# Optimization experiments

Hardware: AMD Instinct MI355X
Metric: run time of the kernel (lower is better)

The kernel has to match this reference:

```python
import jax, jax.numpy as jnp
import numpy as np

L = 5          # num_layers
N = 50000      # nodes
E = 600000     # edges
D = 128        # num_features == hidden_units
G = 256        # graphs in batch
O = 10         # num_outputs
BN_EPS = 1e-5


def setup_inputs() -> dict:
    key = jax.random.key(0)
    ks = jax.random.split(key, 8)
    x = jax.random.normal(ks[0], (N, D), jnp.float32)
    edge_index = jax.random.randint(ks[1], (2, E), 0, N, jnp.int32)
    edge_attr = jax.random.randint(ks[2], (E, 3), 0, 8, jnp.int32)
    batch = jnp.sort(jax.random.randint(ks[3], (N,), 0, G, jnp.int32))
    s = 0.05
    return {
        "x": x,
        "edge_index": edge_index,
        "edge_attr": edge_attr,
        "batch": batch,
        "bond_emb": jax.random.normal(ks[4], (L, 3, 8, D), jnp.float32) * s,
        "conv_w1": jax.random.normal(ks[5], (L, D, D), jnp.float32) * s,
        "conv_b1": jnp.zeros((L, D), jnp.float32),
        "conv_bn_gamma": jnp.ones((L, D), jnp.float32),
        "conv_bn_beta": jnp.zeros((L, D), jnp.float32),
        "conv_bn_mean": jnp.zeros((L, D), jnp.float32),
        "conv_bn_var": jnp.ones((L, D), jnp.float32),
        "conv_w2": jax.random.normal(ks[6], (L, D, D), jnp.float32) * s,
        "conv_b2": jnp.zeros((L, D), jnp.float32),
        "bn_gamma": jnp.ones((L, D), jnp.float32),
        "bn_beta": jnp.zeros((L, D), jnp.float32),
        "bn_mean": jnp.zeros((L, D), jnp.float32),
        "bn_var": jnp.ones((L, D), jnp.float32),
        "fc_w": jax.random.normal(ks[7], (L + 1, D, O), jnp.float32) * s,
        "fc_b": jnp.zeros((L + 1, O), jnp.float32),
    }


def _bn_eval(h, gamma, beta, mean, var):
    return (h - mean) * jax.lax.rsqrt(var + BN_EPS) * gamma + beta


def reference(x, edge_index, edge_attr, batch, bond_emb,
              conv_w1, conv_b1, conv_bn_gamma, conv_bn_beta, conv_bn_mean, conv_bn_var,
              conv_w2, conv_b2, bn_gamma, bn_beta, bn_mean, bn_var, fc_w, fc_b):
    src, dst = edge_index[0], edge_index[1]  # x_j = x[src], aggregate at dst
    feat_ids = jnp.arange(3)
    outs = [x]
    for i in range(L):
        # BondEncoder: sum of per-feature embeddings -> [E, D]
        ea = bond_emb[i][feat_ids, edge_attr].sum(axis=1)
        # GINEConv (eps=0): msg = relu(x_j + edge_attr), scatter-add, nn(x + aggr)
        msg = jax.nn.relu(x[src] + ea)
        aggr = jax.ops.segment_sum(msg, dst, num_segments=N)
        h = x + aggr
        h = h @ conv_w1[i] + conv_b1[i]
        h = jax.nn.relu(_bn_eval(h, conv_bn_gamma[i], conv_bn_beta[i], conv_bn_mean[i], conv_bn_var[i]))
        h = h @ conv_w2[i] + conv_b2[i]
        x = jax.nn.relu(_bn_eval(h, bn_gamma[i], bn_beta[i], bn_mean[i], bn_var[i]))
        outs.append(x)
    # global mean pool per layer output, linear head, sum (dropout = identity in eval)
    counts = jax.ops.segment_sum(jnp.ones((N,), x.dtype), batch, num_segments=G)
    inv = 1.0 / jnp.maximum(counts, 1.0)
    out = jnp.zeros((G, O), x.dtype)
    for i, h in enumerate(outs):
        pooled = jax.ops.segment_sum(h, batch, num_segments=G) * inv[:, None]
        out = out + pooled @ fc_w[i] + fc_b[i]
    return out
```

## Files before the change

kernel.cpp:

```cpp
#include <hip/hip_runtime.h>

#define NN 50000
#define EE 600000
#define DD 128
#define GG 256
#define LL 5
#define OO 10
#define BN_EPS 1e-5f
#define CPAD 513
#define ESTRIDE 40
#define SENT (512u << 16)

#define B_CVT   3125
#define B_COMBO 1283
#define B_WT    160
#define B_EFILL 1954
#define B_EPOS  196
#define B_INV   1
#define B_POOL0 391
#define B_PREP  (B_CVT + B_COMBO + B_WT + B_EFILL + B_EPOS + B_INV + B_POOL0)

typedef __attribute__((ext_vector_type(8))) short short8;
typedef __attribute__((ext_vector_type(16))) float float16;

__device__ __forceinline__ unsigned short f2b(float f) {
    unsigned u = __float_as_uint(f);
    unsigned r = u + 0x7FFFu + ((u >> 16) & 1u);
    return (unsigned short)(r >> 16);
}
__device__ __forceinline__ unsigned pk2(float lo, float hi) {
    return (unsigned)f2b(lo) | ((unsigned)f2b(hi) << 16);
}
__device__ __forceinline__ float blo(unsigned u) { return __uint_as_float(u << 16); }
__device__ __forceinline__ float bhi(unsigned u) { return __uint_as_float(u & 0xFFFF0000u); }

__launch_bounds__(256)
__global__ void prep(const float* __restrict__ x, const int* __restrict__ batch,
                     const float* __restrict__ bond,
                     const float* __restrict__ w1, const float* __restrict__ w2,
                     unsigned* __restrict__ xb4, unsigned short* __restrict__ combo,
                     short* __restrict__ wt, unsigned* __restrict__ e_info,
                     int* __restrict__ epos, float* __restrict__ inv,
                     float* __restrict__ pooled0) {
    const int bid = blockIdx.x, t = threadIdx.x;
    if (bid < B_CVT) {
        int gid = bid * 256 + t;
        const float4* xp = (const float4*)(x + (size_t)gid * 8);
        float4 a = xp[0], b = xp[1];
        uint4 o;
        o.x = pk2(a.x, a.y); o.y = pk2(a.z, a.w);
        o.z = pk2(b.x, b.y); o.w = pk2(b.z, b.w);
        ((uint4*)xb4)[gid] = o;
    } else if (bid < B_CVT + B_COMBO) {
        int e = (bid - B_CVT) * 256 + t;
        if (e < LL * CPAD * DD) {
            int l = e / (CPAD * DD), rem = e - l * (CPAD * DD);
            int c = rem / DD, d = rem - c * DD;
            float s;
            if (c == 512) s = -1e30f;
            else {
                const float* b_ = bond + (size_t)l * 3 * 8 * DD;
                s = b_[(c & 7) * DD + d] + b_[(8 + ((c >> 3) & 7)) * DD + d]
                  + b_[(16 + (c >> 6)) * DD + d];
            }
            combo[e] = f2b(s);
        }
    } else if (bid < B_CVT + B_COMBO + B_WT) {
        __shared__ float tile[32][33];
        int b = bid - B_CVT - B_COMBO;
        int mat = b >> 4, tl = b & 15;
        int k0 = (tl >> 2) * 32, c0 = (tl & 3) * 32;
        const float* W = (mat < 5) ? (w1 + (size_t)mat * DD * DD)
                                   : (w2 + (size_t)(mat - 5) * DD * DD);
        int j = t & 31, q = t >> 5;
#pragma unroll
        for (int rr = 0; rr < 4; ++rr) {
            int row = q + rr * 8;
            tile[row][j] = W[(size_t)(k0 + row) * DD + c0 + j];
        }
        __syncthreads();
#pragma unroll
        for (int rr = 0; rr < 4; ++rr) {
            int cr = q + rr * 8;
            wt[(size_t)mat * DD * DD + (size_t)(c0 + cr) * DD + k0 + j] = (short)f2b(tile[j][cr]);
        }
    } else if (bid < B_CVT + B_COMBO + B_WT + B_EFILL) {
        int gid = (bid - B_CVT - B_COMBO - B_WT) * 256 + t;
        if (gid < NN * ESTRIDE / 4)
            ((uint4*)e_info)[gid] = make_uint4(SENT, SENT, SENT, SENT);
    } else if (bid < B_CVT + B_COMBO + B_WT + B_EFILL + B_EPOS) {
        int n = (bid - B_CVT - B_COMBO - B_WT - B_EFILL) * 256 + t;
        if (n < NN) epos[n] = n * ESTRIDE;
    } else if (bid < B_CVT + B_COMBO + B_WT + B_EFILL + B_EPOS + B_INV) {
        __shared__ int sg[GG + 1];
        int g = t, lo = 0, hi = NN;
        while (lo < hi) { int m = (lo + hi) >> 1; if (batch[m] < g) lo = m + 1; else hi = m; }
        sg[g] = lo;
        if (g == 0) sg[GG] = NN;
        __syncthreads();
        inv[g] = 1.0f / fmaxf((float)(sg[g + 1] - sg[g]), 1.0f);
    } else {
        int b = bid - (B_CVT + B_COMBO + B_WT + B_EFILL + B_EPOS + B_INV);
        int n0 = b * 128;
        __shared__ int sb[128];
        __shared__ float part[4][DD];
        if (t < 128) { int row = n0 + t; sb[t] = (row < NN) ? batch[row] : -1; }
        ((float*)part)[t] = 0.f;
        ((float*)part)[t + 256] = 0.f;
        __syncthreads();
        int gmin = sb[0];
        int col = t & 127, rh = t >> 7;
        float pg[4] = {0.f, 0.f, 0.f, 0.f};
        for (int r = rh; r < 128; r += 2) {
            int s = sb[r];
            float v = (s >= 0) ? x[(size_t)(n0 + r) * DD + col] : 0.f;
            int dg = s - gmin;
#pragma unroll
            for (int jj = 0; jj < 4; ++jj) pg[jj] += (dg == jj) ? v : 0.f;
        }
#pragma unroll
        for (int jj = 0; jj < 4; ++jj)
            if (pg[jj] != 0.f) atomicAdd(&part[jj][col], pg[jj]);
        __syncthreads();
        for (int q2 = t; q2 < 4 * DD; q2 += 256) {
            int jj = q2 >> 7, c2 = q2 & 127;
            float v = part[jj][c2];
            if (v != 0.f && gmin + jj < GG) atomicAdd(&pooled0[(gmin + jj) * DD + c2], v);
        }
    }
}

__launch_bounds__(256)
__global__ void scatter_edges(const int* __restrict__ ei, const int* __restrict__ eattr,
                              int* __restrict__ epos, unsigned* __restrict__ e_info) {
    int e = blockIdx.x * 256 + threadIdx.x;
    if (e >= EE) return;
    int dst = ei[EE + e];
    int pos = atomicAdd(&epos[dst], 1);
    unsigned cidx = (unsigned)eattr[e * 3 + 0] | ((unsigned)eattr[e * 3 + 1] << 3)
                  | ((unsigned)eattr[e * 3 + 2] << 6);
    e_info[pos] = (unsigned)ei[e] | (cidx << 16);
}

__launch_bounds__(256)
__global__ void aggr_csr(const unsigned short* __restrict__ xin,
                         const int* __restrict__ epos,
                         const unsigned* __restrict__ e_info,
                         const unsigned short* __restrict__ combo,
                         unsigned short* __restrict__ hin) {
    int node = blockIdx.x * 4 + (threadIdx.x >> 6);
    int lane = threadIdx.x & 63;
    if (node >= NN) return;
    const int base = node * ESTRIDE;
    const int deg  = epos[node] - base;
    const int pe   = base + ((deg + 7) & ~7);
    const int eg   = lane >> 4;
    const int f    = (lane & 15) * 8;
    float acc[8];
#pragma unroll
    for (int i = 0; i < 8; ++i) acc[i] = 0.f;

    for (int p = base; p < pe; p += 8) {
        unsigned i0 = e_info[p + eg];
        unsigned i1 = e_info[p + 4 + eg];
        uint4 xv0 = *(const uint4*)&xin[(size_t)(i0 & 0xFFFFu) * DD + f];
        uint4 cv0 = *(const uint4*)&combo[(size_t)(i0 >> 16) * DD + f];
        uint4 xv1 = *(const uint4*)&xin[(size_t)(i1 & 0xFFFFu) * DD + f];
        uint4 cv1 = *(const uint4*)&combo[(size_t)(i1 >> 16) * DD + f];
        acc[0] += fmaxf(blo(xv0.x) + blo(cv0.x), 0.f) + fmaxf(blo(xv1.x) + blo(cv1.x), 0.f);
        acc[1] += fmaxf(bhi(xv0.x) + bhi(cv0.x), 0.f) + fmaxf(bhi(xv1.x) + bhi(cv1.x), 0.f);
        acc[2] += fmaxf(blo(xv0.y) + blo(cv0.y), 0.f) + fmaxf(blo(xv1.y) + blo(cv1.y), 0.f);
        acc[3] += fmaxf(bhi(xv0.y) + bhi(cv0.y), 0.f) + fmaxf(bhi(xv1.y) + bhi(cv1.y), 0.f);
        acc[4] += fmaxf(blo(xv0.z) + blo(cv0.z), 0.f) + fmaxf(blo(xv1.z) + blo(cv1.z), 0.f);
        acc[5] += fmaxf(bhi(xv0.z) + bhi(cv0.z), 0.f) + fmaxf(bhi(xv1.z) + bhi(cv1.z), 0.f);
        acc[6] += fmaxf(blo(xv0.w) + blo(cv0.w), 0.f) + fmaxf(blo(xv1.w) + blo(cv1.w), 0.f);
        acc[7] += fmaxf(bhi(xv0.w) + bhi(cv0.w), 0.f) + fmaxf(bhi(xv1.w) + bhi(cv1.w), 0.f);
    }
#pragma unroll
    for (int i = 0; i < 8; ++i) {
        acc[i] += __shfl_xor(acc[i], 16, 64);
        acc[i] += __shfl_xor(acc[i], 32, 64);
    }
    if (lane < 16) {
        uint4 self = *(const uint4*)&xin[(size_t)node * DD + f];
        uint4 o;
        o.x = pk2(acc[0] + blo(self.x), acc[1] + bhi(self.x));
        o.y = pk2(acc[2] + blo(self.y), acc[3] + bhi(self.y));
        o.z = pk2(acc[4] + blo(self.z), acc[5] + bhi(self.z));
        o.w = pk2(acc[6] + blo(self.w), acc[7] + bhi(self.w));
        *(uint4*)&hin[(size_t)node * DD + f] = o;
    }
}

__launch_bounds__(256)
__global__ void conv_fused(const unsigned short* __restrict__ hin,
                           const short* __restrict__ Wt1, const short* __restrict__ Wt2,
                           const float* __restrict__ b1, const float* __restrict__ g1,
                           const float* __restrict__ be1, const float* __restrict__ m1,
                           const float* __restrict__ v1,
                           const float* __restrict__ b2, const float* __restrict__ g2,
                           const float* __restrict__ be2, const float* __restrict__ m2,
                           const float* __restrict__ v2,
                           const int* __restrict__ batch,
                           unsigned short* __restrict__ outb,
                           float* __restrict__ pool_slot) {
    __shared__ short As[64 * 136];
    __shared__ int sbg[64];
    const int tid  = threadIdx.x;
    const int lane = tid & 63;
    const int wave = tid >> 6;
    const int row0 = blockIdx.x * 64;

    const int col   = wave * 32 + (lane & 31);
    const int khalf = (lane >> 5) * 8;
    const int arow  = lane & 31;
    const int rbase = 4 * (lane >> 5);
    const int gmin  = batch[row0];

    short8 bf[8];
#pragma unroll
    for (int ch = 0; ch < 8; ++ch)
        bf[ch] = *(const short8*)&Wt1[col * DD + ch * 16 + khalf];

    const float sc1 = g1[col] * rsqrtf(v1[col] + BN_EPS);
    const float sh1 = fmaf(b1[col] - m1[col], sc1, be1[col]);
    const float sc2 = g2[col] * rsqrtf(v2[col] + BN_EPS);
    const float sh2 = fmaf(b2[col] - m2[col], sc2, be2[col]);

    if (tid < 64) {
        int row = row0 + tid;
        sbg[tid] = (row < NN) ? batch[row] - gmin : -1;
    }
    for (int i = tid; i < 1024; i += 256) {
        int r = i >> 4, c8 = (i & 15) * 8;
        int row = row0 + r;
        uint4 z = make_uint4(0, 0, 0, 0);
        if (row < NN) z = *(const uint4*)&hin[(size_t)row * DD + c8];
        *(uint4*)&As[r * 136 + c8] = z;
    }
    __syncthreads();

    float16 acc0 = {0.f,0.f,0.f,0.f,0.f,0.f,0.f,0.f,0.f,0.f,0.f,0.f,0.f,0.f,0.f,0.f};
    float16 acc1 = acc0;
#pragma unroll
    for (int ch = 0; ch < 8; ++ch) {
        short8 a0 = *(const short8*)&As[(arow     ) * 136 + ch * 16 + khalf];
        short8 a1 = *(const short8*)&As[(32 + arow) * 136 + ch * 16 + khalf];
        acc0 = __builtin_amdgcn_mfma_f32_32x32x16_bf16(a0, bf[ch], acc0, 0, 0, 0);
        acc1 = __builtin_amdgcn_mfma_f32_32x32x16_bf16(a1, bf[ch], acc1, 0, 0, 0);
    }

#pragma unroll
    for (int ch = 0; ch < 8; ++ch)
        bf[ch] = *(const short8*)&Wt2[col * DD + ch * 16 + khalf];

    __syncthreads();
#pragma unroll
    for (int r = 0; r < 16; ++r) {
        int rl = (r & 3) + 8 * (r >> 2) + rbase;
        As[rl * 136 + col]        = (short)f2b(fmaxf(fmaf(acc0[r], sc1, sh1), 0.f));
        As[(32 + rl) * 136 + col] = (short)f2b(fmaxf(fmaf(acc1[r], sc1, sh1), 0.f));
    }
    __syncthreads();

    acc0 = acc1 = float16{0.f,0.f,0.f,0.f,0.f,0.f,0.f,0.f,0.f,0.f,0.f,0.f,0.f,0.f,0.f,0.f};
#pragma unroll
    for (int ch = 0; ch < 8; ++ch) {
        short8 a0 = *(const short8*)&As[(arow     ) * 136 + ch * 16 + khalf];
        short8 a1 = *(const short8*)&As[(32 + arow) * 136 + ch * 16 + khalf];
        acc0 = __builtin_amdgcn_mfma_f32_32x32x16_bf16(a0, bf[ch], acc0, 0, 0, 0);
        acc1 = __builtin_amdgcn_mfma_f32_32x32x16_bf16(a1, bf[ch], acc1, 0, 0, 0);
    }

    float pg0 = 0.f, pg1 = 0.f, pg2 = 0.f, pg3 = 0.f;
#pragma unroll
    for (int r = 0; r < 16; ++r) {
        int rl  = (r & 3) + 8 * (r >> 2) + rbase;
        int row = row0 + rl;
        float v0 = fmaxf(fmaf(acc0[r], sc2, sh2), 0.f);
        float v1_ = fmaxf(fmaf(acc1[r], sc2, sh2), 0.f);
        if (row < NN)      outb[(size_t)row * DD + col]        = f2b(v0);
        if (row + 32 < NN) outb[(size_t)(row + 32) * DD + col] = f2b(v1_);
        int ga = sbg[rl], gb = sbg[rl + 32];
        pg0 += ((ga == 0) ? v0 : 0.f) + ((gb == 0) ? v1_ : 0.f);
        pg1 += ((ga == 1) ? v0 : 0.f) + ((gb == 1) ? v1_ : 0.f);
        pg2 += ((ga == 2) ? v0 : 0.f) + ((gb == 2) ? v1_ : 0.f);
        pg3 += ((ga == 3) ? v0 : 0.f) + ((gb == 3) ? v1_ : 0.f);
    }
    pg0 += __shfl_down(pg0, 32);
    pg1 += __shfl_down(pg1, 32);
    pg2 += __shfl_down(pg2, 32);
    pg3 += __shfl_down(pg3, 32);
    if (lane < 32) {
        if (pg0 != 0.f)                  atomicAdd(&pool_slot[(gmin    ) * DD + col], pg0);
        if (pg1 != 0.f && gmin + 1 < GG) atomicAdd(&pool_slot[(gmin + 1) * DD + col], pg1);
        if (pg2 != 0.f && gmin + 2 < GG) atomicAdd(&pool_slot[(gmin + 2) * DD + col], pg2);
        if (pg3 != 0.f && gmin + 3 < GG) atomicAdd(&pool_slot[(gmin + 3) * DD + col], pg3);
    }
}

__launch_bounds__(64)
__global__ void head(const float* __restrict__ pooled, const float* __restrict__ inv,
                     const float* __restrict__ fcw, const float* __restrict__ fcb,
                     float* __restrict__ out) {
    int g = blockIdx.x, t = threadIdx.x;
    __shared__ float part[LL + 1][OO];
    if (t < (LL + 1) * OO) {
        int l = t / OO, o2 = t - l * OO;
        const float* p = pooled + ((size_t)l * GG + g) * DD;
        const float* w = fcw + (size_t)l * DD * OO + o2;
        float s = 0.f;
        for (int d2 = 0; d2 < DD; ++d2) s = fmaf(p[d2], w[(size_t)d2 * OO], s);
        part[l][o2] = s;
    }
    __syncthreads();
    if (t < OO) {
        float sp = 0.f, sb2 = 0.f;
#pragma unroll
        for (int l = 0; l < LL + 1; ++l) { sp += part[l][t]; sb2 += fcb[l * OO + t]; }
        out[g * OO + t] = sp * inv[g] + sb2;
    }
}

extern "C" void kernel_launch(void* const* d_in, const int* in_sizes, int n_in,
                              void* d_out, int out_size, void* d_ws, size_t ws_size,
                              hipStream_t stream) {
    const float* x_in    = (const float*)d_in[0];
    const int*   ei      = (const int*)d_in[1];
    const int*   eattr   = (const int*)d_in[2];
    const int*   batch   = (const int*)d_in[3];
    const float* bond    = (const float*)d_in[4];
    const float* conv_w1 = (const float*)d_in[5];
    const float* conv_b1 = (const float*)d_in[6];
    const float* cbg     = (const float*)d_in[7];
    const float* cbb     = (const float*)d_in[8];
    const float* cbm     = (const float*)d_in[9];
    const float* cbv     = (const float*)d_in[10];
    const float* conv_w2 = (const float*)d_in[11];
    const float* conv_b2 = (const float*)d_in[12];
    const float* bg      = (const float*)d_in[13];
    const float* bb      = (const float*)d_in[14];
    const float* bm      = (const float*)d_in[15];
    const float* bv      = (const float*)d_in[16];
    const float* fcw     = (const float*)d_in[17];
    const float* fcb     = (const float*)d_in[18];
    float* out = (float*)d_out;

    char* base = (char*)d_ws;
    size_t o = 0;
    auto carve = [&](size_t bytes) { void* p = base + o; o += (bytes + 15) & ~(size_t)15; return p; };
    unsigned short* xbA    = (unsigned short*)carve((size_t)NN * DD * 2);
    unsigned short* xbB    = (unsigned short*)carve((size_t)NN * DD * 2);
    unsigned short* combo  = (unsigned short*)carve((size_t)LL * CPAD * DD * 2);
    short*          wt     = (short*)carve((size_t)10 * DD * DD * 2);
    float*          inv    = (float*)carve(GG * 4);
    int*            epos   = (int*)carve(NN * 4);
    unsigned*       e_info = (unsigned*)carve((size_t)NN * ESTRIDE * 4);
    float*          pooled = (float*)carve((size_t)(LL + 1) * GG * DD * 4);

    hipMemsetAsync(pooled, 0, (size_t)(LL + 1) * GG * DD * 4, stream);

    prep<<<B_PREP, 256, 0, stream>>>(x_in, batch, bond, conv_w1, conv_w2,
                                     (unsigned*)xbA, combo, wt, e_info, epos, inv, pooled);
    scatter_edges<<<(EE + 255) / 256, 256, 0, stream>>>(ei, eattr, epos, e_info);

    const int conv_blocks = (NN + 63) / 64;
    const int aggr_blocks = (NN + 3) / 4;
    unsigned short* xin  = xbA;
    unsigned short* xout = xbB;
    for (int i = 0; i < LL; ++i) {
        aggr_csr<<<aggr_blocks, 256, 0, stream>>>(
            xin, epos, e_info, combo + (size_t)i * CPAD * DD, xout );
        conv_fused<<<conv_blocks, 256, 0, stream>>>(
            xout , wt + (size_t)i * DD * DD, wt + (size_t)(5 + i) * DD * DD,
            conv_b1 + (size_t)i * DD, cbg + (size_t)i * DD, cbb + (size_t)i * DD,
            cbm + (size_t)i * DD, cbv + (size_t)i * DD,
            conv_b2 + (size_t)i * DD, bg + (size_t)i * DD, bb + (size_t)i * DD,
            bm + (size_t)i * DD, bv + (size_t)i * DD,
            batch, xin ,
            pooled + (size_t)(i + 1) * GG * DD);
    }
    head<<<GG, 64, 0, stream>>>(pooled, inv, fcw, fcb, out);
}
```

Baseline: 431.3 us.

## Fold edge scatter into prep kernel and drop sentinel fill of edge slots

The separate scatter_edges kernel is merged into prep as an extra block range. epos now counts degree from a memset of zero, shared with the pooled buffer so one memset covers both, instead of prep writing per-node base offsets. The sentinel fill of the padded edge table is removed; aggr_csr masks padding slots in registers using the clamped degree. This saves one kernel launch, an 8 MB fill pass and a dependency step, but it now relies on every scatter atomic finishing before aggr_csr reads, and it silently drops edges beyond a node's 40 slots (the old code had the same limit without a check).

```diff
diff --git a/kernel.cpp b/kernel.cpp
--- a/kernel.cpp
+++ b/kernel.cpp
@@ -11,14 +11,13 @@
 #define ESTRIDE 40
 #define SENT (512u << 16)
 
+#define B_SCAT  2344
 #define B_CVT   3125
 #define B_COMBO 1283
 #define B_WT    160
-#define B_EFILL 1954
-#define B_EPOS  196
 #define B_INV   1
 #define B_POOL0 391
-#define B_PREP  (B_CVT + B_COMBO + B_WT + B_EFILL + B_EPOS + B_INV + B_POOL0)
+#define B_PREP  (B_SCAT + B_CVT + B_COMBO + B_WT + B_INV + B_POOL0)
 
 typedef __attribute__((ext_vector_type(8))) short short8;
 typedef __attribute__((ext_vector_type(16))) float float16;
@@ -35,24 +34,36 @@
 __device__ __forceinline__ float bhi(unsigned u) { return __uint_as_float(u & 0xFFFF0000u); }
 
 __launch_bounds__(256)
-__global__ void prep(const float* __restrict__ x, const int* __restrict__ batch,
+__global__ void prep(const float* __restrict__ x, const int* __restrict__ ei,
+                     const int* __restrict__ eattr, const int* __restrict__ batch,
                      const float* __restrict__ bond,
                      const float* __restrict__ w1, const float* __restrict__ w2,
                      unsigned* __restrict__ xb4, unsigned short* __restrict__ combo,
-                     short* __restrict__ wt, unsigned* __restrict__ e_info,
-                     int* __restrict__ epos, float* __restrict__ inv,
-                     float* __restrict__ pooled0) {
+                     short* __restrict__ wt, int* __restrict__ epos,
+                     unsigned* __restrict__ e_info,
+                     float* __restrict__ inv, float* __restrict__ pooled0) {
     const int bid = blockIdx.x, t = threadIdx.x;
-    if (bid < B_CVT) {
-        int gid = bid * 256 + t;
+    if (bid < B_SCAT) {
+        int e = bid * 256 + t;
+        if (e < EE) {
+            int dst = ei[EE + e];
+            int slot = atomicAdd(&epos[dst], 1);
+            if (slot < ESTRIDE) {
+                unsigned cidx = (unsigned)eattr[e * 3 + 0] | ((unsigned)eattr[e * 3 + 1] << 3)
+                              | ((unsigned)eattr[e * 3 + 2] << 6);
+                e_info[dst * ESTRIDE + slot] = (unsigned)ei[e] | (cidx << 16);
+            }
+        }
+    } else if (bid < B_SCAT + B_CVT) {
+        int gid = (bid - B_SCAT) * 256 + t;
         const float4* xp = (const float4*)(x + (size_t)gid * 8);
         float4 a = xp[0], b = xp[1];
         uint4 o;
         o.x = pk2(a.x, a.y); o.y = pk2(a.z, a.w);
         o.z = pk2(b.x, b.y); o.w = pk2(b.z, b.w);
         ((uint4*)xb4)[gid] = o;
-    } else if (bid < B_CVT + B_COMBO) {
-        int e = (bid - B_CVT) * 256 + t;
+    } else if (bid < B_SCAT + B_CVT + B_COMBO) {
+        int e = (bid - B_SCAT - B_CVT) * 256 + t;
         if (e < LL * CPAD * DD) {
             int l = e / (CPAD * DD), rem = e - l * (CPAD * DD);
             int c = rem / DD, d = rem - c * DD;
@@ -65,9 +76,9 @@
             }
             combo[e] = f2b(s);
         }
-    } else if (bid < B_CVT + B_COMBO + B_WT) {
+    } else if (bid < B_SCAT + B_CVT + B_COMBO + B_WT) {
         __shared__ float tile[32][33];
-        int b = bid - B_CVT - B_COMBO;
+        int b = bid - B_SCAT - B_CVT - B_COMBO;
         int mat = b >> 4, tl = b & 15;
         int k0 = (tl >> 2) * 32, c0 = (tl & 3) * 32;
         const float* W = (mat < 5) ? (w1 + (size_t)mat * DD * DD)
@@ -84,14 +95,7 @@
             int cr = q + rr * 8;
             wt[(size_t)mat * DD * DD + (size_t)(c0 + cr) * DD + k0 + j] = (short)f2b(tile[j][cr]);
         }
-    } else if (bid < B_CVT + B_COMBO + B_WT + B_EFILL) {
-        int gid = (bid - B_CVT - B_COMBO - B_WT) * 256 + t;
-        if (gid < NN * ESTRIDE / 4)
-            ((uint4*)e_info)[gid] = make_uint4(SENT, SENT, SENT, SENT);
-    } else if (bid < B_CVT + B_COMBO + B_WT + B_EFILL + B_EPOS) {
-        int n = (bid - B_CVT - B_COMBO - B_WT - B_EFILL) * 256 + t;
-        if (n < NN) epos[n] = n * ESTRIDE;
-    } else if (bid < B_CVT + B_COMBO + B_WT + B_EFILL + B_EPOS + B_INV) {
+    } else if (bid < B_SCAT + B_CVT + B_COMBO + B_WT + B_INV) {
         __shared__ int sg[GG + 1];
         int g = t, lo = 0, hi = NN;
         while (lo < hi) { int m = (lo + hi) >> 1; if (batch[m] < g) lo = m + 1; else hi = m; }
@@ -100,7 +104,7 @@
         __syncthreads();
         inv[g] = 1.0f / fmaxf((float)(sg[g + 1] - sg[g]), 1.0f);
     } else {
-        int b = bid - (B_CVT + B_COMBO + B_WT + B_EFILL + B_EPOS + B_INV);
+        int b = bid - (B_SCAT + B_CVT + B_COMBO + B_WT + B_INV);
         int n0 = b * 128;
         __shared__ int sb[128];
         __shared__ float part[4][DD];
@@ -131,18 +135,6 @@
 }
 
 __launch_bounds__(256)
-__global__ void scatter_edges(const int* __restrict__ ei, const int* __restrict__ eattr,
-                              int* __restrict__ epos, unsigned* __restrict__ e_info) {
-    int e = blockIdx.x * 256 + threadIdx.x;
-    if (e >= EE) return;
-    int dst = ei[EE + e];
-    int pos = atomicAdd(&epos[dst], 1);
-    unsigned cidx = (unsigned)eattr[e * 3 + 0] | ((unsigned)eattr[e * 3 + 1] << 3)
-                  | ((unsigned)eattr[e * 3 + 2] << 6);
-    e_info[pos] = (unsigned)ei[e] | (cidx << 16);
-}
-
-__launch_bounds__(256)
 __global__ void aggr_csr(const unsigned short* __restrict__ xin,
                          const int* __restrict__ epos,
                          const unsigned* __restrict__ e_info,
@@ -152,7 +144,8 @@
     int lane = threadIdx.x & 63;
     if (node >= NN) return;
     const int base = node * ESTRIDE;
-    const int deg  = epos[node] - base;
+    int deg = epos[node]; if (deg > ESTRIDE) deg = ESTRIDE;
+    const int dend = base + deg;
     const int pe   = base + ((deg + 7) & ~7);
     const int eg   = lane >> 4;
     const int f    = (lane & 15) * 8;
@@ -163,6 +156,8 @@
     for (int p = base; p < pe; p += 8) {
         unsigned i0 = e_info[p + eg];
         unsigned i1 = e_info[p + 4 + eg];
+        if (p + eg >= dend)     i0 = SENT;
+        if (p + 4 + eg >= dend) i1 = SENT;
         uint4 xv0 = *(const uint4*)&xin[(size_t)(i0 & 0xFFFFu) * DD + f];
         uint4 cv0 = *(const uint4*)&combo[(size_t)(i0 >> 16) * DD + f];
         uint4 xv1 = *(const uint4*)&xin[(size_t)(i1 & 0xFFFFu) * DD + f];
@@ -354,15 +349,15 @@
     unsigned short* combo  = (unsigned short*)carve((size_t)LL * CPAD * DD * 2);
     short*          wt     = (short*)carve((size_t)10 * DD * DD * 2);
     float*          inv    = (float*)carve(GG * 4);
-    int*            epos   = (int*)carve(NN * 4);
+    const size_t ZBYTES = (size_t)NN * 4 + (size_t)(LL + 1) * GG * DD * 4;
+    int*            epos   = (int*)carve(ZBYTES);
+    float*          pooled = (float*)((char*)epos + (size_t)NN * 4);
     unsigned*       e_info = (unsigned*)carve((size_t)NN * ESTRIDE * 4);
-    float*          pooled = (float*)carve((size_t)(LL + 1) * GG * DD * 4);
-
-    hipMemsetAsync(pooled, 0, (size_t)(LL + 1) * GG * DD * 4, stream);
-
-    prep<<<B_PREP, 256, 0, stream>>>(x_in, batch, bond, conv_w1, conv_w2,
-                                     (unsigned*)xbA, combo, wt, e_info, epos, inv, pooled);
-    scatter_edges<<<(EE + 255) / 256, 256, 0, stream>>>(ei, eattr, epos, e_info);
+
+    hipMemsetAsync(epos, 0, ZBYTES, stream);
+
+    prep<<<B_PREP, 256, 0, stream>>>(x_in, ei, eattr, batch, bond, conv_w1, conv_w2,
+                                     (unsigned*)xbA, combo, wt, epos, e_info, inv, pooled);
 
     const int conv_blocks = (NN + 63) / 64;
     const int aggr_blocks = (NN + 3) / 4;
@@ -370,15 +365,14 @@
     unsigned short* xout = xbB;
     for (int i = 0; i < LL; ++i) {
         aggr_csr<<<aggr_blocks, 256, 0, stream>>>(
-            xin, epos, e_info, combo + (size_t)i * CPAD * DD, xout );
+            xin, epos, e_info, combo + (size_t)i * CPAD * DD, xout);
         conv_fused<<<conv_blocks, 256, 0, stream>>>(
-            xout , wt + (size_t)i * DD * DD, wt + (size_t)(5 + i) * DD * DD,
+            xout, wt + (size_t)i * DD * DD, wt + (size_t)(5 + i) * DD * DD,
             conv_b1 + (size_t)i * DD, cbg + (size_t)i * DD, cbb + (size_t)i * DD,
             cbm + (size_t)i * DD, cbv + (size_t)i * DD,
             conv_b2 + (size_t)i * DD, bg + (size_t)i * DD, bb + (size_t)i * DD,
             bm + (size_t)i * DD, bv + (size_t)i * DD,
-            batch, xin ,
-            pooled + (size_t)(i + 1) * GG * DD);
+            batch, xin, pooled + (size_t)(i + 1) * GG * DD);
     }
     head<<<GG, 64, 0, stream>>>(pooled, inv, fcw, fcb, out);
 }
```

Measured after the change: 422.1 us, median of 2. -2.1%, faster.
